# Performance work log

Measured on AMD Instinct MI355X. Metric: run time of the kernel, lower is better.

Reference implementation:

```python
import jax, jax.numpy as jnp
import numpy as np

B, S, D, H = 2, 2048, 768, 12
HD = D // H


def setup_inputs() -> dict:
    key = jax.random.key(0)
    ks = jax.random.split(key, 6)
    sc = 1.0 / np.sqrt(D)
    return {
        "x": jax.random.normal(ks[0], (B, S, D), dtype=jnp.float32),
        "mask": jnp.tril(jnp.ones((S, S), dtype=jnp.int32)),  # causal GPT mask
        "Wq": jax.random.normal(ks[1], (D, D), dtype=jnp.float32) * sc,
        "bq": jnp.zeros((D,), dtype=jnp.float32),
        "Wk": jax.random.normal(ks[2], (D, D), dtype=jnp.float32) * sc,
        "bk": jnp.zeros((D,), dtype=jnp.float32),
        "Wv": jax.random.normal(ks[3], (D, D), dtype=jnp.float32) * sc,
        "bv": jnp.zeros((D,), dtype=jnp.float32),
        "Wo": jax.random.normal(ks[4], (D, D), dtype=jnp.float32) * sc,
        "bo": jnp.zeros((D,), dtype=jnp.float32),
    }


def reference(x, mask, Wq, bq, Wk, bk, Wv, bv, Wo, bo):
    # Linear projections (torch Linear: x @ W.T + b; here W stored as [in,out])
    Q = (x @ Wq + bq).reshape(B, S, H, HD).transpose(0, 2, 1, 3)  # [B,H,S,HD]
    K = (x @ Wk + bk).reshape(B, S, H, HD).transpose(0, 2, 1, 3)
    V = (x @ Wv + bv).reshape(B, S, H, HD).transpose(0, 2, 1, 3)

    scores = jnp.einsum('bhqd,bhkd->bhqk', Q, K) / jnp.sqrt(jnp.float32(HD))
    scores = jnp.where(mask[None, None, :, :] == 0, jnp.float32(-1e9), scores)
    attn_weights = jax.nn.softmax(scores, axis=-1)  # dropout is identity in eval
    attn_out = jnp.einsum('bhqk,bhkd->bhqd', attn_weights, V)

    attn_out = attn_out.transpose(0, 2, 1, 3).reshape(B, S, D)
    out = attn_out @ Wo + bo
    return out, attn_weights
```

## Files before the change

### kernel.cpp

```cpp
#include <hip/hip_runtime.h>

#define DEV static __device__ __forceinline__

typedef __bf16 bf16x8 __attribute__((ext_vector_type(8)));
typedef float  f32x4  __attribute__((ext_vector_type(4)));

DEV bf16x8 ld8(const __bf16* p) { return *reinterpret_cast<const bf16x8*>(p); }

DEV f32x4 mfma16(bf16x8 a, bf16x8 b, f32x4 c) {
  return __builtin_amdgcn_mfma_f32_16x16x32_bf16(a, b, c, 0, 0, 0);
}

#define SEQ 2048
#define DIM 768
#define NH  12
#define HDIM 64

DEV void decode_chunk2(int cid, int CH, int& qt, int& t0) {
  int q = 0, rem = cid;
  while (true) {
    int nc = (2 * q + 2 + CH - 1) / CH;
    if (rem < nc) break;
    rem -= nc; ++q;
  }
  qt = q; t0 = rem * CH;
}

__global__ __launch_bounds__(256) void prep_misc(const float* __restrict__ x,
                                                 __bf16* __restrict__ xb,
                                                 float* __restrict__ zp) {
  const int bid = blockIdx.x, tid = threadIdx.x;
  if (bid < 1024) {
    const int n4 = (3145728 + 49152) / 4;
    const f32x4 zv = {0.f, 0.f, 0.f, 0.f};
    for (int i = bid * 256 + tid; i < n4; i += 1024 * 256) ((f32x4*)zp)[i] = zv;
  } else {
    const int i = ((bid - 1024) * 256 + tid) * 8;
    f32x4 a = *(const f32x4*)(x + i);
    f32x4 b = *(const f32x4*)(x + i + 4);
    bf16x8 v;
    #pragma unroll
    for (int j = 0; j < 4; ++j) { v[j] = (__bf16)a[j]; v[4 + j] = (__bf16)b[j]; }
    *(bf16x8*)(xb + i) = v;
  }
}

__global__ __launch_bounds__(256) void prep_wt(
    const float* __restrict__ Wq, const float* __restrict__ Wk,
    const float* __restrict__ Wv, const float* __restrict__ Wo,
    __bf16* __restrict__ WbT) {
  __shared__ float T[64][65];
  const int z = blockIdx.z;
  const float* W = (z == 0) ? Wq : (z == 1) ? Wk : (z == 2) ? Wv : Wo;
  const int kb = blockIdx.x * 64, nb = blockIdx.y * 64;
  const int t = threadIdx.x, r = t >> 2, c4 = (t & 3) * 16;
  #pragma unroll
  for (int j = 0; j < 16; j += 4) {
    f32x4 v = *(const f32x4*)(W + (size_t)(kb + r) * DIM + nb + c4 + j);
    T[r][c4 + j]     = v[0]; T[r][c4 + j + 1] = v[1];
    T[r][c4 + j + 2] = v[2]; T[r][c4 + j + 3] = v[3];
  }
  __syncthreads();
  bf16x8 o0, o1;
  #pragma unroll
  for (int j = 0; j < 8; ++j) {
    o0[j] = (__bf16)T[c4 + j][r];
    o1[j] = (__bf16)T[c4 + 8 + j][r];
  }
  __bf16* dst = WbT + (size_t)z * DIM * DIM + (size_t)(nb + r) * DIM + kb + c4;
  *(bf16x8*)dst = o0;
  *(bf16x8*)(dst + 8) = o1;
}

DEV void gemm128(const __bf16* __restrict__ Ab, const __bf16* __restrict__ Bt,
                 const float* __restrict__ bias, void* __restrict__ outp,
                 const int mode, const float scale,
                 const int mbase, const int nbase) {
  __shared__ __bf16 As[128][72];
  __shared__ __bf16 Bs[128][72];

  const int tid  = threadIdx.x;
  const int l    = tid & 63;
  const int w    = tid >> 6;
  const int lrow = l & 15;
  const int lk8  = (l >> 4) * 8;
  const int wr = (w >> 1) * 64, wc = (w & 1) * 64;

  f32x4 acc[4][4] = {};

  const int srow = tid >> 1;
  const int scol = (tid & 1) * 32;

  for (int kk = 0; kk < DIM; kk += 64) {
    {
      const __bf16* a = Ab + (size_t)(mbase + srow) * DIM + kk + scol;
      *(bf16x8*)&As[srow][scol]      = ld8(a);
      *(bf16x8*)&As[srow][scol + 8]  = ld8(a + 8);
      *(bf16x8*)&As[srow][scol + 16] = ld8(a + 16);
      *(bf16x8*)&As[srow][scol + 24] = ld8(a + 24);
    }
    {
      const __bf16* b = Bt + (size_t)(nbase + srow) * DIM + kk + scol;
      *(bf16x8*)&Bs[srow][scol]      = ld8(b);
      *(bf16x8*)&Bs[srow][scol + 8]  = ld8(b + 8);
      *(bf16x8*)&Bs[srow][scol + 16] = ld8(b + 16);
      *(bf16x8*)&Bs[srow][scol + 24] = ld8(b + 24);
    }
    __syncthreads();
    #pragma unroll
    for (int kc = 0; kc < 2; ++kc) {
      bf16x8 af[4], bf[4];
      #pragma unroll
      for (int mi = 0; mi < 4; ++mi)
        af[mi] = ld8(&As[wr + mi * 16 + lrow][kc * 32 + lk8]);
      #pragma unroll
      for (int ni = 0; ni < 4; ++ni)
        bf[ni] = ld8(&Bs[wc + ni * 16 + lrow][kc * 32 + lk8]);
      #pragma unroll
      for (int mi = 0; mi < 4; ++mi)
        #pragma unroll
        for (int ni = 0; ni < 4; ++ni)
          acc[mi][ni] = mfma16(af[mi], bf[ni], acc[mi][ni]);
    }
    __syncthreads();
  }

  #pragma unroll
  for (int mi = 0; mi < 4; ++mi)
  #pragma unroll
  for (int ni = 0; ni < 4; ++ni) {
    const int n  = nbase + wc + ni * 16 + lrow;
    const float bn = bias[n];
    const int hh = n >> 6, hd = n & 63;
    #pragma unroll
    for (int r = 0; r < 4; ++r) {
      const int m = mbase + wr + mi * 16 + (l >> 4) * 4 + r;
      const float v = (acc[mi][ni][r] + bn) * scale;
      const int bb = m >> 11, s = m & (SEQ - 1);
      if (mode == 0) {
        ((__bf16*)outp)[(((size_t)(bb * NH + hh) * SEQ) + s) * HDIM + hd] = (__bf16)v;
      } else {
        ((__bf16*)outp)[(((size_t)(bb * NH + hh) * HDIM) + hd) * SEQ + s] = (__bf16)v;
      }
    }
  }
}

__global__ __launch_bounds__(256, 2) void qkv_gemm(
    const __bf16* __restrict__ xb, const __bf16* __restrict__ WbT,
    const float* __restrict__ bq, const float* __restrict__ bk,
    const float* __restrict__ bv,
    __bf16* __restrict__ Qb, __bf16* __restrict__ Kb, __bf16* __restrict__ Vt) {
  const int z = blockIdx.z;
  const __bf16* Bt = WbT + (size_t)z * DIM * DIM;
  const float* bs = (z == 0) ? bq : (z == 1) ? bk : bv;
  void* o = (z == 0) ? (void*)Qb : (z == 1) ? (void*)Kb : (void*)Vt;
  const float sc = (z == 0) ? 0.125f : 1.f;
  gemm128(xb, Bt, bs, o, (z == 2) ? 1 : 0, sc,
          blockIdx.y * 128, blockIdx.x * 128);
}

__global__ __launch_bounds__(256, 4) void out_gemm(
    const float* __restrict__ Af, const __bf16* __restrict__ WbT,
    const float* __restrict__ bias, float* __restrict__ out) {
  __shared__ __bf16 As[64][72];
  __shared__ __bf16 Bs[64][72];

  const __bf16* Bt = WbT + (size_t)3 * DIM * DIM;
  const int mbase = blockIdx.y * 64, nbase = blockIdx.x * 64;
  const int tid  = threadIdx.x;
  const int l    = tid & 63;
  const int w    = tid >> 6;
  const int lrow = l & 15;
  const int lk8  = (l >> 4) * 8;
  const int wrow = (w >> 1) * 32, wcol = (w & 1) * 32;

  f32x4 acc[2][2] = {};

  const int arow = tid >> 2;
  const int acol = (tid & 3) * 16;

  for (int kk = 0; kk < DIM; kk += 64) {
    {
      const float* src = Af + (size_t)(mbase + arow) * DIM + kk + acol;
      f32x4 f0 = *(const f32x4*)(src);
      f32x4 f1 = *(const f32x4*)(src + 4);
      f32x4 f2 = *(const f32x4*)(src + 8);
      f32x4 f3 = *(const f32x4*)(src + 12);
      bf16x8 v0, v1;
      #pragma unroll
      for (int j = 0; j < 4; ++j) {
        v0[j] = (__bf16)f0[j]; v0[4 + j] = (__bf16)f1[j];
        v1[j] = (__bf16)f2[j]; v1[4 + j] = (__bf16)f3[j];
      }
      *(bf16x8*)&As[arow][acol]     = v0;
      *(bf16x8*)&As[arow][acol + 8] = v1;
    }
    {
      const __bf16* bsrc = Bt + (size_t)(nbase + arow) * DIM + kk + acol;
      *(bf16x8*)&Bs[arow][acol]     = ld8(bsrc);
      *(bf16x8*)&Bs[arow][acol + 8] = ld8(bsrc + 8);
    }
    __syncthreads();
    #pragma unroll
    for (int kc = 0; kc < 2; ++kc) {
      bf16x8 a0 = ld8(&As[wrow + lrow][kc * 32 + lk8]);
      bf16x8 a1 = ld8(&As[wrow + 16 + lrow][kc * 32 + lk8]);
      bf16x8 b0 = ld8(&Bs[wcol + lrow][kc * 32 + lk8]);
      bf16x8 b1 = ld8(&Bs[wcol + 16 + lrow][kc * 32 + lk8]);
      acc[0][0] = mfma16(a0, b0, acc[0][0]);
      acc[0][1] = mfma16(a0, b1, acc[0][1]);
      acc[1][0] = mfma16(a1, b0, acc[1][0]);
      acc[1][1] = mfma16(a1, b1, acc[1][1]);
    }
    __syncthreads();
  }

  #pragma unroll
  for (int mi = 0; mi < 2; ++mi)
  #pragma unroll
  for (int ni = 0; ni < 2; ++ni) {
    const int n  = nbase + wcol + ni * 16 + lrow;
    const float bn = bias[n];
    #pragma unroll
    for (int r = 0; r < 4; ++r) {
      const int m = mbase + wrow + mi * 16 + (l >> 4) * 4 + r;
      out[(size_t)m * DIM + n] = acc[mi][ni][r] + bn;
    }
  }
}

__global__ __launch_bounds__(256, 4) void attn_sums(
    const __bf16* __restrict__ Q, const __bf16* __restrict__ K,
    float* __restrict__ sums, float* __restrict__ Wout) {
  const int tid = threadIdx.x, l = tid & 63, w = tid >> 6;
  const int lrow = l & 15, lk8 = (l >> 4) * 8, g = l >> 4;
  const int lin = blockIdx.x;
  const int C = 72;
  const int bh = (lin & 7) * 3 + (lin >> 3) / C;
  const int cid = (lin >> 3) % C;
  int qt, t0; decode_chunk2(cid, 4, qt, t0);
  const int tmax = 2 * qt + 2;
  const int t1 = (t0 + 4 < tmax) ? t0 + 4 : tmax;
  const int fb0 = qt * 128 + w * 32;
  const int fb1 = fb0 + 16;
  const int q0 = fb0 + lrow, q1 = fb1 + lrow;

  const __bf16* Qh = Q + (size_t)bh * SEQ * HDIM;
  const __bf16* Kh = K + (size_t)bh * SEQ * HDIM;
  const bf16x8 bqA0 = ld8(Qh + (size_t)q0 * HDIM + lk8);
  const bf16x8 bqA1 = ld8(Qh + (size_t)q0 * HDIM + 32 + lk8);
  const bf16x8 bqB0 = ld8(Qh + (size_t)q1 * HDIM + lk8);
  const bf16x8 bqB1 = ld8(Qh + (size_t)q1 * HDIM + 32 + lk8);

  float sA = 0.f, sB = 0.f;
  for (int t = t0; t < t1; ++t) {
    const int kb = t * 64;
    const bool liveA = (kb <= fb0 + 15);
    const bool liveB = (kb <= fb1 + 15);
    if (!liveB) continue;
    #pragma unroll
    for (int nt = 0; nt < 4; ++nt) {
      const int krow = kb + nt * 16 + lrow;
      const bf16x8 ak0 = ld8(Kh + (size_t)krow * HDIM + lk8);
      const bf16x8 ak1 = ld8(Kh + (size_t)krow * HDIM + 32 + lk8);
      const int k0 = kb + nt * 16 + g * 4;
      if (liveA) {
        f32x4 s0 = {0.f, 0.f, 0.f, 0.f}, s1 = {0.f, 0.f, 0.f, 0.f};
        s0 = mfma16(ak0, bqA0, s0);
        s1 = mfma16(ak1, bqA1, s1);
        if (kb + 63 <= fb0) {
          #pragma unroll
          for (int r = 0; r < 4; ++r) sA += __expf(s0[r] + s1[r]);
        } else {
          #pragma unroll
          for (int r = 0; r < 4; ++r)
            sA += (k0 + r <= q0) ? __expf(s0[r] + s1[r]) : 0.f;
        }
      }
      {
        f32x4 s0 = {0.f, 0.f, 0.f, 0.f}, s1 = {0.f, 0.f, 0.f, 0.f};
        s0 = mfma16(ak0, bqB0, s0);
        s1 = mfma16(ak1, bqB1, s1);
        if (kb + 63 <= fb1) {
          #pragma unroll
          for (int r = 0; r < 4; ++r) sB += __expf(s0[r] + s1[r]);
        } else {
          #pragma unroll
          for (int r = 0; r < 4; ++r)
            sB += (k0 + r <= q1) ? __expf(s0[r] + s1[r]) : 0.f;
        }
      }
    }
  }
  sA += __shfl_xor(sA, 16); sA += __shfl_xor(sA, 32);
  sB += __shfl_xor(sB, 16); sB += __shfl_xor(sB, 32);
  if (g == 0) {
    unsafeAtomicAdd(&sums[bh * SEQ + q0], sA);
    unsafeAtomicAdd(&sums[bh * SEQ + q1], sB);
  }

  const int tz = (t1 < 2 * qt) ? t1 : 2 * qt;
  if (t0 < tz) {
    float* Wg = Wout + (size_t)bh * SEQ * SEQ;
    const int zr = tid >> 2;
    const int zc = (tid & 3) * 32;
    const f32x4 zv = {0.f, 0.f, 0.f, 0.f};
    for (int t = t0; t < tz; ++t) {
      float* base = Wg + (size_t)(t * 64 + zr) * SEQ + qt * 128 + zc;
      #pragma unroll
      for (int c = 0; c < 8; ++c) *(f32x4*)(base + c * 4) = zv;
    }
  }
}

__global__ __launch_bounds__(256, 4) void attn_wpv(
    const __bf16* __restrict__ Q, const __bf16* __restrict__ K,
    const __bf16* __restrict__ VT, const float* __restrict__ sums,
    float* __restrict__ Wout, float* __restrict__ AOf) {
  __shared__ float Plds[4][2][16][68];

  const int tid = threadIdx.x, l = tid & 63, w = tid >> 6;
  const int lrow = l & 15, lk8 = (l >> 4) * 8, g = l >> 4;
  const int lin = blockIdx.x;
  const int C = 40;
  const int bh = (lin & 7) * 3 + (lin >> 3) / C;
  const int cid = (lin >> 3) % C;
  int qt, t0; decode_chunk2(cid, 8, qt, t0);
  const int tmax = 2 * qt + 2;
  const int t1 = (t0 + 8 < tmax) ? t0 + 8 : tmax;
  const int bb = bh / NH, hh = bh % NH;
  const int fb0 = qt * 128 + w * 32;
  const int fb1 = fb0 + 16;
  const int q0 = fb0 + lrow, q1 = fb1 + lrow;

  const __bf16* Qh = Q + (size_t)bh * SEQ * HDIM;
  const __bf16* Kh = K + (size_t)bh * SEQ * HDIM;
  const __bf16* Vh = VT + (size_t)bh * HDIM * SEQ;
  float* Wg = Wout + (size_t)bh * SEQ * SEQ;

  const bf16x8 bqA0 = ld8(Qh + (size_t)q0 * HDIM + lk8);
  const bf16x8 bqA1 = ld8(Qh + (size_t)q0 * HDIM + 32 + lk8);
  const bf16x8 bqB0 = ld8(Qh + (size_t)q1 * HDIM + lk8);
  const bf16x8 bqB1 = ld8(Qh + (size_t)q1 * HDIM + 32 + lk8);
  const float invA = 1.f / sums[bh * SEQ + q0];
  const float invB = 1.f / sums[bh * SEQ + q1];

  f32x4 accA[4] = {}, accB[4] = {};
  for (int t = t0; t < t1; ++t) {
    const int kb = t * 64;
    const bool liveA = (kb <= fb0 + 15);
    const bool liveB = (kb <= fb1 + 15);
    const f32x4 zv = {0.f, 0.f, 0.f, 0.f};
    if (!liveB) {
      #pragma unroll
      for (int nt = 0; nt < 4; ++nt) {
        const int k0 = kb + nt * 16 + g * 4;
        *(f32x4*)&Wg[(size_t)q0 * SEQ + k0] = zv;
        *(f32x4*)&Wg[(size_t)q1 * SEQ + k0] = zv;
      }
      continue;
    }
    #pragma unroll
    for (int nt = 0; nt < 4; ++nt) {
      const int krow = kb + nt * 16 + lrow;
      const bf16x8 ak0 = ld8(Kh + (size_t)krow * HDIM + lk8);
      const bf16x8 ak1 = ld8(Kh + (size_t)krow * HDIM + 32 + lk8);
      const int k0 = kb + nt * 16 + g * 4;
      f32x4 pvA = zv;
      if (liveA) {
        f32x4 s0 = {0.f, 0.f, 0.f, 0.f}, s1 = {0.f, 0.f, 0.f, 0.f};
        s0 = mfma16(ak0, bqA0, s0);
        s1 = mfma16(ak1, bqA1, s1);
        if (kb + 63 <= fb0) {
          #pragma unroll
          for (int r = 0; r < 4; ++r) pvA[r] = __expf(s0[r] + s1[r]) * invA;
        } else {
          #pragma unroll
          for (int r = 0; r < 4; ++r)
            pvA[r] = (k0 + r <= q0) ? __expf(s0[r] + s1[r]) * invA : 0.f;
        }
        *(f32x4*)&Plds[w][0][lrow][nt * 16 + g * 4] = pvA;
      }
      *(f32x4*)&Wg[(size_t)q0 * SEQ + k0] = pvA;
      f32x4 pvB;
      {
        f32x4 s0 = {0.f, 0.f, 0.f, 0.f}, s1 = {0.f, 0.f, 0.f, 0.f};
        s0 = mfma16(ak0, bqB0, s0);
        s1 = mfma16(ak1, bqB1, s1);
        if (kb + 63 <= fb1) {
          #pragma unroll
          for (int r = 0; r < 4; ++r) pvB[r] = __expf(s0[r] + s1[r]) * invB;
        } else {
          #pragma unroll
          for (int r = 0; r < 4; ++r)
            pvB[r] = (k0 + r <= q1) ? __expf(s0[r] + s1[r]) * invB : 0.f;
        }
      }
      *(f32x4*)&Wg[(size_t)q1 * SEQ + k0] = pvB;
      *(f32x4*)&Plds[w][1][lrow][nt * 16 + g * 4] = pvB;
    }
    #pragma unroll
    for (int kc = 0; kc < 2; ++kc) {
      bf16x8 awA, awB;
      if (liveA) {
        const float* ps = &Plds[w][0][lrow][kc * 32 + lk8];
        const f32x4 p0 = *(const f32x4*)ps;
        const f32x4 p1 = *(const f32x4*)(ps + 4);
        #pragma unroll
        for (int j = 0; j < 4; ++j) { awA[j] = (__bf16)p0[j]; awA[4 + j] = (__bf16)p1[j]; }
      }
      {
        const float* ps = &Plds[w][1][lrow][kc * 32 + lk8];
        const f32x4 p0 = *(const f32x4*)ps;
        const f32x4 p1 = *(const f32x4*)(ps + 4);
        #pragma unroll
        for (int j = 0; j < 4; ++j) { awB[j] = (__bf16)p0[j]; awB[4 + j] = (__bf16)p1[j]; }
      }
      #pragma unroll
      for (int nt = 0; nt < 4; ++nt) {
        const bf16x8 bv =
            ld8(Vh + (size_t)(nt * 16 + lrow) * SEQ + kb + kc * 32 + lk8);
        if (liveA) accA[nt] = mfma16(awA, bv, accA[nt]);
        accB[nt] = mfma16(awB, bv, accB[nt]);
      }
    }
  }

  #pragma unroll
  for (int nt = 0; nt < 4; ++nt)
    #pragma unroll
    for (int r = 0; r < 4; ++r) {
      unsafeAtomicAdd(
          &AOf[(size_t)(bb * SEQ + fb0 + g * 4 + r) * DIM + hh * HDIM + nt * 16 + lrow],
          accA[nt][r]);
      unsafeAtomicAdd(
          &AOf[(size_t)(bb * SEQ + fb1 + g * 4 + r) * DIM + hh * HDIM + nt * 16 + lrow],
          accB[nt][r]);
    }
}

extern "C" void kernel_launch(void* const* d_in, const int* in_sizes, int n_in,
                              void* d_out, int out_size, void* d_ws, size_t ws_size,
                              hipStream_t stream) {
  const float* x  = (const float*)d_in[0];
  const float* Wq = (const float*)d_in[2];
  const float* bq = (const float*)d_in[3];
  const float* Wk = (const float*)d_in[4];
  const float* bk = (const float*)d_in[5];
  const float* Wv = (const float*)d_in[6];
  const float* bv = (const float*)d_in[7];
  const float* Wo = (const float*)d_in[8];
  const float* bo = (const float*)d_in[9];

  char* wsb = (char*)d_ws;
  __bf16* Qb   = (__bf16*)(wsb);
  __bf16* Kb   = (__bf16*)(wsb + 6291456);
  __bf16* Vt   = (__bf16*)(wsb + 12582912);
  float*  AOf  = (float*)(wsb + 18874368);
  float*  sums = (float*)(wsb + 31457280);
  __bf16* WbT  = (__bf16*)(wsb + 31653888);

  float* out   = (float*)d_out;
  float* attnW = out + 3145728;
  __bf16* xb   = (__bf16*)attnW;

  prep_misc<<<2560, 256, 0, stream>>>(x, xb, AOf);
  prep_wt<<<dim3(12, 12, 4), 256, 0, stream>>>(Wq, Wk, Wv, Wo, WbT);
  qkv_gemm<<<dim3(6, 32, 3), 256, 0, stream>>>(xb, WbT, bq, bk, bv, Qb, Kb, Vt);
  attn_sums<<<1728, 256, 0, stream>>>(Qb, Kb, sums, attnW);
  attn_wpv<<<960, 256, 0, stream>>>(Qb, Kb, Vt, sums, attnW, AOf);
  out_gemm<<<dim3(12, 64), 256, 0, stream>>>(AOf, WbT, bo, out);
}
```

Before: 274.2 us.

## Enlarge attn_sums query tile to 256 rows and stage P in LDS as bf16

```diff
diff --git a/kernel.cpp b/kernel.cpp
--- a/kernel.cpp
+++ b/kernel.cpp
@@ -3,6 +3,7 @@
 #define DEV static __device__ __forceinline__
 
 typedef __bf16 bf16x8 __attribute__((ext_vector_type(8)));
+typedef __bf16 bf16x4 __attribute__((ext_vector_type(4)));
 typedef float  f32x4  __attribute__((ext_vector_type(4)));
 
 DEV bf16x8 ld8(const __bf16* p) { return *reinterpret_cast<const bf16x8*>(p); }
@@ -24,6 +25,12 @@
     rem -= nc; ++q;
   }
   qt = q; t0 = rem * CH;
+}
+
+DEV void decode_chunk4(int cid, int& st, int& t0) {
+  int q = 0, rem = cid;
+  while (rem >= q + 1) { rem -= q + 1; ++q; }
+  st = q; t0 = rem * 4;
 }
 
 __global__ __launch_bounds__(256) void prep_misc(const float* __restrict__ x,
@@ -236,78 +243,85 @@
   const int tid = threadIdx.x, l = tid & 63, w = tid >> 6;
   const int lrow = l & 15, lk8 = (l >> 4) * 8, g = l >> 4;
   const int lin = blockIdx.x;
-  const int C = 72;
+  const int C = 36;
   const int bh = (lin & 7) * 3 + (lin >> 3) / C;
   const int cid = (lin >> 3) % C;
-  int qt, t0; decode_chunk2(cid, 4, qt, t0);
-  const int tmax = 2 * qt + 2;
+  int st, t0; decode_chunk4(cid, st, t0);
+  const int tmax = 4 * st + 4;
   const int t1 = (t0 + 4 < tmax) ? t0 + 4 : tmax;
-  const int fb0 = qt * 128 + w * 32;
-  const int fb1 = fb0 + 16;
-  const int q0 = fb0 + lrow, q1 = fb1 + lrow;
 
   const __bf16* Qh = Q + (size_t)bh * SEQ * HDIM;
   const __bf16* Kh = K + (size_t)bh * SEQ * HDIM;
-  const bf16x8 bqA0 = ld8(Qh + (size_t)q0 * HDIM + lk8);
-  const bf16x8 bqA1 = ld8(Qh + (size_t)q0 * HDIM + 32 + lk8);
-  const bf16x8 bqB0 = ld8(Qh + (size_t)q1 * HDIM + lk8);
-  const bf16x8 bqB1 = ld8(Qh + (size_t)q1 * HDIM + 32 + lk8);
-
-  float sA = 0.f, sB = 0.f;
+
+  int fb[4];
+  bf16x8 bq0[4], bq1[4];
+  #pragma unroll
+  for (int i = 0; i < 4; ++i) {
+    fb[i] = st * 256 + w * 64 + i * 16;
+    const int q = fb[i] + lrow;
+    bq0[i] = ld8(Qh + (size_t)q * HDIM + lk8);
+    bq1[i] = ld8(Qh + (size_t)q * HDIM + 32 + lk8);
+  }
+
+  float ssum[4] = {0.f, 0.f, 0.f, 0.f};
   for (int t = t0; t < t1; ++t) {
     const int kb = t * 64;
-    const bool liveA = (kb <= fb0 + 15);
-    const bool liveB = (kb <= fb1 + 15);
-    if (!liveB) continue;
+    if (kb > fb[3] + 15) continue;
     #pragma unroll
     for (int nt = 0; nt < 4; ++nt) {
       const int krow = kb + nt * 16 + lrow;
       const bf16x8 ak0 = ld8(Kh + (size_t)krow * HDIM + lk8);
       const bf16x8 ak1 = ld8(Kh + (size_t)krow * HDIM + 32 + lk8);
       const int k0 = kb + nt * 16 + g * 4;
-      if (liveA) {
-        f32x4 s0 = {0.f, 0.f, 0.f, 0.f}, s1 = {0.f, 0.f, 0.f, 0.f};
-        s0 = mfma16(ak0, bqA0, s0);
-        s1 = mfma16(ak1, bqA1, s1);
-        if (kb + 63 <= fb0) {
-          #pragma unroll
-          for (int r = 0; r < 4; ++r) sA += __expf(s0[r] + s1[r]);
-        } else {
-          #pragma unroll
-          for (int r = 0; r < 4; ++r)
-            sA += (k0 + r <= q0) ? __expf(s0[r] + s1[r]) : 0.f;
+      #pragma unroll
+      for (int i = 0; i < 4; ++i) {
+        if (kb <= fb[i] + 15) {
+          f32x4 s0 = {0.f, 0.f, 0.f, 0.f}, s1 = {0.f, 0.f, 0.f, 0.f};
+          s0 = mfma16(ak0, bq0[i], s0);
+          s1 = mfma16(ak1, bq1[i], s1);
+          const int q = fb[i] + lrow;
+          if (kb + 63 <= fb[i]) {
+            #pragma unroll
+            for (int r = 0; r < 4; ++r) ssum[i] += __expf(s0[r] + s1[r]);
+          } else {
+            #pragma unroll
+            for (int r = 0; r < 4; ++r)
+              ssum[i] += (k0 + r <= q) ? __expf(s0[r] + s1[r]) : 0.f;
+          }
         }
       }
-      {
-        f32x4 s0 = {0.f, 0.f, 0.f, 0.f}, s1 = {0.f, 0.f, 0.f, 0.f};
-        s0 = mfma16(ak0, bqB0, s0);
-        s1 = mfma16(ak1, bqB1, s1);
-        if (kb + 63 <= fb1) {
-          #pragma unroll
-          for (int r = 0; r < 4; ++r) sB += __expf(s0[r] + s1[r]);
-        } else {
-          #pragma unroll
-          for (int r = 0; r < 4; ++r)
-            sB += (k0 + r <= q1) ? __expf(s0[r] + s1[r]) : 0.f;
-        }
-      }
-    }
-  }
-  sA += __shfl_xor(sA, 16); sA += __shfl_xor(sA, 32);
-  sB += __shfl_xor(sB, 16); sB += __shfl_xor(sB, 32);
+    }
+  }
+  #pragma unroll
+  for (int i = 0; i < 4; ++i) {
+    ssum[i] += __shfl_xor(ssum[i], 16);
+    ssum[i] += __shfl_xor(ssum[i], 32);
+  }
   if (g == 0) {
-    unsafeAtomicAdd(&sums[bh * SEQ + q0], sA);
-    unsafeAtomicAdd(&sums[bh * SEQ + q1], sB);
-  }
-
-  const int tz = (t1 < 2 * qt) ? t1 : 2 * qt;
+    #pragma unroll
+    for (int i = 0; i < 4; ++i)
+      unsafeAtomicAdd(&sums[bh * SEQ + fb[i] + lrow], ssum[i]);
+  }
+
+  float* Wg = Wout + (size_t)bh * SEQ * SEQ;
+  const f32x4 zv = {0.f, 0.f, 0.f, 0.f};
+  const int tz = (t1 < 4 * st) ? t1 : 4 * st;
   if (t0 < tz) {
-    float* Wg = Wout + (size_t)bh * SEQ * SEQ;
+    const int zr = tid >> 2;
+    const int zc = (tid & 3) * 64;
+    for (int t = t0; t < tz; ++t) {
+      float* base = Wg + (size_t)(t * 64 + zr) * SEQ + st * 256 + zc;
+      #pragma unroll
+      for (int c = 0; c < 16; ++c) *(f32x4*)(base + c * 4) = zv;
+    }
+  }
+  const int ta = (t0 > 4 * st) ? t0 : 4 * st;
+  const int tb = (t1 < 4 * st + 2) ? t1 : 4 * st + 2;
+  if (ta < tb) {
     const int zr = tid >> 2;
     const int zc = (tid & 3) * 32;
-    const f32x4 zv = {0.f, 0.f, 0.f, 0.f};
-    for (int t = t0; t < tz; ++t) {
-      float* base = Wg + (size_t)(t * 64 + zr) * SEQ + qt * 128 + zc;
+    for (int t = ta; t < tb; ++t) {
+      float* base = Wg + (size_t)(t * 64 + zr) * SEQ + st * 256 + 128 + zc;
       #pragma unroll
       for (int c = 0; c < 8; ++c) *(f32x4*)(base + c * 4) = zv;
     }
@@ -318,7 +332,7 @@
     const __bf16* __restrict__ Q, const __bf16* __restrict__ K,
     const __bf16* __restrict__ VT, const float* __restrict__ sums,
     float* __restrict__ Wout, float* __restrict__ AOf) {
-  __shared__ float Plds[4][2][16][68];
+  __shared__ __bf16 Plds[4][2][16][72];
 
   const int tid = threadIdx.x, l = tid & 63, w = tid >> 6;
   const int lrow = l & 15, lk8 = (l >> 4) * 8, g = l >> 4;
@@ -380,7 +394,10 @@
           for (int r = 0; r < 4; ++r)
             pvA[r] = (k0 + r <= q0) ? __expf(s0[r] + s1[r]) * invA : 0.f;
         }
-        *(f32x4*)&Plds[w][0][lrow][nt * 16 + g * 4] = pvA;
+        bf16x4 pb;
+        #pragma unroll
+        for (int r = 0; r < 4; ++r) pb[r] = (__bf16)pvA[r];
+        *(bf16x4*)&Plds[w][0][lrow][nt * 16 + g * 4] = pb;
       }
       *(f32x4*)&Wg[(size_t)q0 * SEQ + k0] = pvA;
       f32x4 pvB;
@@ -398,25 +415,16 @@
         }
       }
       *(f32x4*)&Wg[(size_t)q1 * SEQ + k0] = pvB;
-      *(f32x4*)&Plds[w][1][lrow][nt * 16 + g * 4] = pvB;
+      bf16x4 pb;
+      #pragma unroll
+      for (int r = 0; r < 4; ++r) pb[r] = (__bf16)pvB[r];
+      *(bf16x4*)&Plds[w][1][lrow][nt * 16 + g * 4] = pb;
     }
     #pragma unroll
     for (int kc = 0; kc < 2; ++kc) {
       bf16x8 awA, awB;
-      if (liveA) {
-        const float* ps = &Plds[w][0][lrow][kc * 32 + lk8];
-        const f32x4 p0 = *(const f32x4*)ps;
-        const f32x4 p1 = *(const f32x4*)(ps + 4);
-        #pragma unroll
-        for (int j = 0; j < 4; ++j) { awA[j] = (__bf16)p0[j]; awA[4 + j] = (__bf16)p1[j]; }
-      }
-      {
-        const float* ps = &Plds[w][1][lrow][kc * 32 + lk8];
-        const f32x4 p0 = *(const f32x4*)ps;
-        const f32x4 p1 = *(const f32x4*)(ps + 4);
-        #pragma unroll
-        for (int j = 0; j < 4; ++j) { awB[j] = (__bf16)p0[j]; awB[4 + j] = (__bf16)p1[j]; }
-      }
+      if (liveA) awA = ld8(&Plds[w][0][lrow][kc * 32 + lk8]);
+      awB = ld8(&Plds[w][1][lrow][kc * 32 + lk8]);
       #pragma unroll
       for (int nt = 0; nt < 4; ++nt) {
         const bf16x8 bv =
@@ -468,7 +476,7 @@
   prep_misc<<<2560, 256, 0, stream>>>(x, xb, AOf);
   prep_wt<<<dim3(12, 12, 4), 256, 0, stream>>>(Wq, Wk, Wv, Wo, WbT);
   qkv_gemm<<<dim3(6, 32, 3), 256, 0, stream>>>(xb, WbT, bq, bk, bv, Qb, Kb, Vt);
-  attn_sums<<<1728, 256, 0, stream>>>(Qb, Kb, sums, attnW);
+  attn_sums<<<864, 256, 0, stream>>>(Qb, Kb, sums, attnW);
   attn_wpv<<<960, 256, 0, stream>>>(Qb, Kb, Vt, sums, attnW, AOf);
   out_gemm<<<dim3(12, 64), 256, 0, stream>>>(AOf, WbT, bo, out);
 }
```

Result: no change. 270.1 us (median of 2 runs) (-1.5%).
